# Kernel optimization log

Measured on AMD Instinct MI355X. Metric: run time of the kernel, lower is better.

The kernel has to match this reference:

```python
import jax, jax.numpy as jnp
import numpy as np

BETA = 0.25
EPS = 1e-12

def normalise(x):
    # L2 normalise over last axis
    return x / jnp.sqrt(jnp.sum(x * x, axis=-1, keepdims=True) + EPS)

def setup_inputs() -> dict:
    key = jax.random.key(0)
    k = jax.random.split(key, 6)
    N, d, c, P = 8192, 768, 256, 16384
    return {
        "z": jax.random.normal(k[0], (N, d), dtype=jnp.float32),
        "W_in": jax.random.normal(k[1], (d, c), dtype=jnp.float32) * 0.02,
        "b_in": jnp.zeros((c,), dtype=jnp.float32),
        "W_out": jax.random.normal(k[2], (c, d), dtype=jnp.float32) * 0.02,
        "b_out": jnp.zeros((d,), dtype=jnp.float32),
        "codebook": jax.random.normal(k[3], (P, c), dtype=jnp.float32),
    }

def reference(z, W_in, b_in, W_out, b_out, codebook):
    sg = jax.lax.stop_gradient
    # input projection + L2 normalise
    zq = normalise(z @ W_in + b_in)                 # [N, c]
    cb = normalise(codebook)                        # [P, c]
    # squared euclidean distances: ||z||^2 - 2 z.c + ||c||^2
    dist = (jnp.sum(zq * zq, axis=-1, keepdims=True)
            - 2.0 * jnp.einsum('nc,pc->np', zq, cb)
            + jnp.sum(cb * cb, axis=-1)[None, :])   # [N, P]
    idxes = jnp.argmin(dist, axis=-1)               # [N]
    codes = normalise(codebook[idxes])              # gather + normalise, [N, c]
    loss = BETA * (zq - sg(codes)) ** 2 + (sg(zq) - codes) ** 2
    # straight-through estimator
    codes = zq + sg(codes - zq)
    out = codes @ W_out + b_out                     # [N, d]
    return out, loss, idxes
```

## Files before the change

kernel.cpp:

```cpp
#include <hip/hip_runtime.h>
#include <hip/hip_fp16.h>
#include <math.h>

#define NN 8192
#define DD 768
#define CC 256
#define PP 16384
#define NG 256
#define MARGIN 5.0e-3f
#define BETA_C 1.25f
#define EPS_C 1e-12f

typedef __attribute__((ext_vector_type(8))) _Float16 f16x8;
typedef __attribute__((ext_vector_type(8))) short bf16x8;
typedef __attribute__((ext_vector_type(4))) float f32x4;
typedef __attribute__((ext_vector_type(16))) float f32x16;

static __device__ __forceinline__ ushort f2h(float x) {
    _Float16 h = (_Float16)x;
    return __builtin_bit_cast(unsigned short, h);
}
static __device__ __forceinline__ ushort f2bf(float x) {
    unsigned u = __float_as_uint(x);
    return (ushort)((u + 0x7fffu + ((u >> 16) & 1u)) >> 16);
}

static __device__ __forceinline__ void gload_lds16(const void* g, void* l) {
    __builtin_amdgcn_global_load_lds(
        (const __attribute__((address_space(1))) unsigned int*)g,
        (__attribute__((address_space(3))) unsigned int*)l, 16, 0, 0);
}

__global__ __launch_bounds__(256) void k_gemm_in(const float* __restrict__ z,
    const float* __restrict__ W, const float* __restrict__ b,
    float* __restrict__ zq)
{
    __shared__ float zt[64][36];
    __shared__ float wt[32][68];
    const int t = threadIdx.x;
    const int ti = t >> 4, tj = t & 15;
    const int n0 = blockIdx.x * 64;
    const int c0 = blockIdx.y * 64;

    f32x4 acc[4];
#pragma unroll
    for (int r = 0; r < 4; ++r) acc[r] = (f32x4){0.f, 0.f, 0.f, 0.f};

    for (int k0 = 0; k0 < DD; k0 += 32) {
        __syncthreads();
#pragma unroll
        for (int l = 0; l < 2; ++l) {
            int idx = l * 256 + t;
            int row = idx >> 3, c4 = idx & 7;
            *reinterpret_cast<float4*>(&zt[row][c4 * 4]) =
                *reinterpret_cast<const float4*>(&z[(size_t)(n0 + row) * DD + k0 + c4 * 4]);
            int krow = idx >> 4, w4 = idx & 15;
            *reinterpret_cast<float4*>(&wt[krow][w4 * 4]) =
                *reinterpret_cast<const float4*>(&W[(size_t)(k0 + krow) * CC + c0 + w4 * 4]);
        }
        __syncthreads();
#pragma unroll
        for (int kk = 0; kk < 32; kk += 4) {
            float4 a4[4], b4[4];
#pragma unroll
            for (int r = 0; r < 4; ++r)
                a4[r] = *reinterpret_cast<const float4*>(&zt[ti * 4 + r][kk]);
#pragma unroll
            for (int q = 0; q < 4; ++q)
                b4[q] = *reinterpret_cast<const float4*>(&wt[kk + q][tj * 4]);
#pragma unroll
            for (int q = 0; q < 4; ++q)
#pragma unroll
                for (int r = 0; r < 4; ++r) {
                    float av = ((const float*)&a4[r])[q];
                    acc[r].x += av * b4[q].x;
                    acc[r].y += av * b4[q].y;
                    acc[r].z += av * b4[q].z;
                    acc[r].w += av * b4[q].w;
                }
        }
    }
#pragma unroll
    for (int r = 0; r < 4; ++r) {
        int col = c0 + tj * 4;
        float4 o;
        o.x = acc[r].x + b[col];
        o.y = acc[r].y + b[col + 1];
        o.z = acc[r].z + b[col + 2];
        o.w = acc[r].w + b[col + 3];
        *reinterpret_cast<float4*>(&zq[(size_t)(n0 + ti * 4 + r) * CC + col]) = o;
    }
}

__global__ __launch_bounds__(256) void k_norm2(const float* __restrict__ src,
    float* __restrict__ dstf32, ushort* __restrict__ dsth, int rows)
{
    const int wave = threadIdx.x >> 6;
    const int lane = threadIdx.x & 63;
    const int row = blockIdx.x * 4 + wave;
    if (row >= rows) return;
    float4 v = *reinterpret_cast<const float4*>(&src[(size_t)row * CC + lane * 4]);
    float s = v.x * v.x + v.y * v.y + v.z * v.z + v.w * v.w;
#pragma unroll
    for (int off = 32; off; off >>= 1) s += __shfl_xor(s, off, 64);
    float r = 1.0f / sqrtf(s + EPS_C);
    v.x *= r; v.y *= r; v.z *= r; v.w *= r;
    *reinterpret_cast<float4*>(&dstf32[(size_t)row * CC + lane * 4]) = v;
    ushort4 hv;
    hv.x = f2h(v.x); hv.y = f2h(v.y); hv.z = f2h(v.z); hv.w = f2h(v.w);
    *reinterpret_cast<ushort4*>(&dsth[(size_t)row * CC + lane * 4]) = hv;
}

__global__ __launch_bounds__(256) void k_prep(const float* __restrict__ codebook,
    ushort* __restrict__ cbh, float* __restrict__ cz2, float* __restrict__ rinv,
    const float* __restrict__ W, ushort* __restrict__ wthi)
{
    __shared__ float tile[64][68];
    const int t = threadIdx.x;
    if (blockIdx.x < 4096) {
        const int wave = t >> 6;
        const int lane = t & 63;
        const int row = blockIdx.x * 4 + wave;
        float4 v = *reinterpret_cast<const float4*>(&codebook[(size_t)row * CC + lane * 4]);
        float s = v.x * v.x + v.y * v.y + v.z * v.z + v.w * v.w;
#pragma unroll
        for (int off = 32; off; off >>= 1) s += __shfl_xor(s, off, 64);
        float r = 1.0f / sqrtf(s + EPS_C);
        v.x *= r; v.y *= r; v.z *= r; v.w *= r;
        ushort4 hv;
        hv.x = f2h(v.x); hv.y = f2h(v.y); hv.z = f2h(v.z); hv.w = f2h(v.w);
        *reinterpret_cast<ushort4*>(&cbh[(size_t)row * CC + lane * 4]) = hv;
        float s2 = v.x * v.x + v.y * v.y + v.z * v.z + v.w * v.w;
#pragma unroll
        for (int off = 32; off; off >>= 1) s2 += __shfl_xor(s2, off, 64);
        if (lane == 0) {
            cz2[row] = s2;
            rinv[row] = r;
        }
    } else {
        const int id = blockIdx.x - 4096;
        const int d0 = (id % 12) * 64;
        const int k0 = (id / 12) * 64;
#pragma unroll
        for (int i = 0; i < 16; ++i) {
            int row = i * 4 + (t >> 6);
            int col = t & 63;
            tile[row][col] = W[(size_t)(k0 + row) * DD + d0 + col];
        }
        __syncthreads();
#pragma unroll
        for (int i = 0; i < 16; ++i) {
            int drow = i * 4 + (t >> 6);
            int kc = t & 63;
            wthi[(size_t)(d0 + drow) * CC + k0 + kc] = f2bf(tile[kc][drow]);
        }
    }
}

__global__ __launch_bounds__(256) void k_dist(
    const ushort* __restrict__ cbh, const ushort* __restrict__ zqh,
    const float* __restrict__ cz2,
    float* __restrict__ gmin, unsigned long long* __restrict__ maskA)
{
    __shared__ ushort lds[2][12288];
    const int t = threadIdx.x;
    const int lane = t & 63;
    const int w = t >> 6;
    const int wr = w >> 1;
    const int wc = w & 1;
    const int p0 = blockIdx.x * 256;
    const int n0 = blockIdx.y * 128;
    const int kh = lane >> 5;
    const int r31 = lane & 31;

    f32x16 acc[4][2];
#pragma unroll
    for (int mi = 0; mi < 4; ++mi) {
        const int pbm = p0 + wr * 128 + mi * 32;
#pragma unroll
        for (int q = 0; q < 4; ++q) {
            float4 cz = *reinterpret_cast<const float4*>(&cz2[pbm + q * 8 + kh * 4]);
#pragma unroll
            for (int j = 0; j < 4; ++j) {
                float v = -0.5f * ((const float*)&cz.x)[j];
                acc[mi][0][q * 4 + j] = v;
                acc[mi][1][q * 4 + j] = v;
            }
        }
    }

    const int u_l = lane >> 3;
    const int e = (lane & 7) ^ u_l;
    const int hh = e >> 2, jj = e & 3;
    const ushort* srcA[4];
    const ushort* srcB[2];
#pragma unroll
    for (int i = 0; i < 4; ++i)
        srcA[i] = cbh + (size_t)(p0 + 2 * (w * 32 + i * 8 + u_l) + hh) * CC + jj * 8;
#pragma unroll
    for (int i = 0; i < 2; ++i)
        srcB[i] = zqh + (size_t)(n0 + 2 * (w * 16 + i * 8 + u_l) + hh) * CC + jj * 8;

#define STAGE(BUF, KT)                                                        \
    {                                                                         \
        _Pragma("unroll")                                                     \
        for (int i = 0; i < 4; ++i)                                           \
            gload_lds16(srcA[i] + (KT) * 32, &lds[BUF][(w * 32 + i * 8) * 64]); \
        _Pragma("unroll")                                                     \
        for (int i = 0; i < 2; ++i)                                           \
            gload_lds16(srcB[i] + (KT) * 32, &lds[BUF][8192 + (w * 16 + i * 8) * 64]); \
    }

    const int ua = wr * 64 + (r31 >> 1);
    const int ub = wc * 32 + (r31 >> 1);
    const int hb = (r31 & 1) * 4 + kh;

#define COMPUTE(BUF)                                                          \
    {                                                                         \
        _Pragma("unroll")                                                     \
        for (int ks = 0; ks < 2; ++ks) {                                      \
            f16x8 af[4], bfv[2];                                              \
            _Pragma("unroll")                                                 \
            for (int mi = 0; mi < 4; ++mi) {                                  \
                int u = ua + mi * 16;                                         \
                af[mi] = *reinterpret_cast<const f16x8*>(                     \
                    &lds[BUF][u * 64 + (((hb + ks * 2) ^ (u & 7)) * 8)]);     \
            }                                                                 \
            _Pragma("unroll")                                                 \
            for (int ni = 0; ni < 2; ++ni) {                                  \
                int u = ub + ni * 16;                                         \
                bfv[ni] = *reinterpret_cast<const f16x8*>(                    \
                    &lds[BUF][8192 + u * 64 + (((hb + ks * 2) ^ (u & 7)) * 8)]); \
            }                                                                 \
            __builtin_amdgcn_s_setprio(1);                                    \
            acc[0][0] = __builtin_amdgcn_mfma_f32_32x32x16_f16(af[0], bfv[0], acc[0][0], 0, 0, 0); \
            acc[0][1] = __builtin_amdgcn_mfma_f32_32x32x16_f16(af[0], bfv[1], acc[0][1], 0, 0, 0); \
            acc[1][0] = __builtin_amdgcn_mfma_f32_32x32x16_f16(af[1], bfv[0], acc[1][0], 0, 0, 0); \
            acc[1][1] = __builtin_amdgcn_mfma_f32_32x32x16_f16(af[1], bfv[1], acc[1][1], 0, 0, 0); \
            acc[2][0] = __builtin_amdgcn_mfma_f32_32x32x16_f16(af[2], bfv[0], acc[2][0], 0, 0, 0); \
            acc[2][1] = __builtin_amdgcn_mfma_f32_32x32x16_f16(af[2], bfv[1], acc[2][1], 0, 0, 0); \
            acc[3][0] = __builtin_amdgcn_mfma_f32_32x32x16_f16(af[3], bfv[0], acc[3][0], 0, 0, 0); \
            acc[3][1] = __builtin_amdgcn_mfma_f32_32x32x16_f16(af[3], bfv[1], acc[3][1], 0, 0, 0); \
            __builtin_amdgcn_s_setprio(0);                                    \
        }                                                                     \
    }

#define BODY(KT, VM, DOSTAGE)                                                 \
    {                                                                         \
        if (DOSTAGE) STAGE(((KT) + 1) & 1, (KT) + 1);                         \
        __builtin_amdgcn_sched_barrier(0);                                    \
        asm volatile("s_waitcnt vmcnt(" #VM ")" ::: "memory");                \
        __builtin_amdgcn_s_barrier();                                         \
        __builtin_amdgcn_sched_barrier(0);                                    \
        COMPUTE((KT) & 1);                                                    \
        if ((KT) < 7) __builtin_amdgcn_s_barrier();                           \
    }

    STAGE(0, 0);
    BODY(0, 6, 1)
    BODY(1, 6, 1)
    BODY(2, 6, 1)
    BODY(3, 6, 1)
    BODY(4, 6, 1)
    BODY(5, 6, 1)
    BODY(6, 6, 1)
    BODY(7, 0, 0)

#undef BODY
#undef COMPUTE
#undef STAGE

#pragma unroll
    for (int ni = 0; ni < 2; ++ni) {
#pragma unroll
        for (int g = 0; g < 2; ++g) {
            float M = -1e30f;
#pragma unroll
            for (int m2 = 0; m2 < 2; ++m2)
#pragma unroll
                for (int r = 0; r < 16; ++r) M = fmaxf(M, acc[g * 2 + m2][ni][r]);
            M = fmaxf(M, __shfl_xor(M, 32, 64));
            const float thr = M - 0.5f * MARGIN;
            unsigned long long msk = 0ull;
#pragma unroll
            for (int m2 = 0; m2 < 2; ++m2)
#pragma unroll
                for (int q = 0; q < 4; ++q) {
                    unsigned nib = 0u;
#pragma unroll
                    for (int j = 0; j < 4; ++j)
                        nib |= (acc[g * 2 + m2][ni][q * 4 + j] >= thr) ? (1u << j) : 0u;
                    msk |= (unsigned long long)nib << (m2 * 32 + q * 8 + kh * 4);
                }
            msk |= __shfl_xor(msk, 32, 64);
            if (kh == 0) {
                int n = n0 + wc * 64 + ni * 32 + r31;
                int grp = (p0 >> 6) + wr * 2 + g;
                gmin[(size_t)n * NG + grp] = -2.0f * M;
                maskA[(size_t)n * NG + grp] = msk;
            }
        }
    }
}

__global__ __launch_bounds__(256) void k_pick(
    const float* __restrict__ gmin, const unsigned long long* __restrict__ maskA,
    const float* __restrict__ zqn, const float* __restrict__ cb_raw,
    const float* __restrict__ rinv, const float* __restrict__ cz2,
    float* __restrict__ idxf, ushort* __restrict__ chi, float* __restrict__ loss)
{
    __shared__ int lst[4][256];
    __shared__ int cnt[4];
    const int t = threadIdx.x;
    const int w = t >> 6;
    const int lane = t & 63;
    const int row = blockIdx.x * 4 + w;

    float4 zr = *reinterpret_cast<const float4*>(&zqn[(size_t)row * CC + lane * 4]);
    float4 gv = *reinterpret_cast<const float4*>(&gmin[(size_t)row * NG + lane * 4]);

    float pm = fminf(fminf(gv.x, gv.y), fminf(gv.z, gv.w));
#pragma unroll
    for (int off = 1; off < 64; off <<= 1) pm = fminf(pm, __shfl_xor(pm, off, 64));
    const float thresh = pm + MARGIN;

    if (lane == 0) cnt[w] = 0;
    __syncthreads();
    {
        const float g4[4] = {gv.x, gv.y, gv.z, gv.w};
#pragma unroll
        for (int j = 0; j < 4; ++j)
            if (g4[j] <= thresh) {
                int pos = atomicAdd(&cnt[w], 1);
                lst[w][pos] = lane * 4 + j;
            }
    }
    __syncthreads();

    const int nc = cnt[w];
    unsigned long long best = ~0ull;
    for (int ci = 0; ci < nc; ++ci) {
        int g = lst[w][ci];
        unsigned long long msk = maskA[(size_t)row * NG + g];
        while (msk) {
            int bit = __ffsll((long long)msk) - 1;
            msk &= msk - 1;
            int p = g * 64 + bit;
            float rv = rinv[p];
            float4 c4 = *reinterpret_cast<const float4*>(&cb_raw[(size_t)p * CC + lane * 4]);
            float part = (c4.x * rv) * zr.x + (c4.y * rv) * zr.y
                       + (c4.z * rv) * zr.z + (c4.w * rv) * zr.w;
#pragma unroll
            for (int off = 1; off < 64; off <<= 1) part += __shfl_xor(part, off, 64);
            float d4 = fmaf(-2.0f, part, 4.0f + cz2[p]);
            unsigned long long pk = ((unsigned long long)__float_as_uint(d4) << 32) | (unsigned)p;
            best = best < pk ? best : pk;
        }
    }
    const int p = (int)(best & 0xffffffffu);
    if (lane == 0) idxf[row] = (float)p;

    const float rv = rinv[p];
    float4 cv = *reinterpret_cast<const float4*>(&cb_raw[(size_t)p * CC + lane * 4]);
    cv.x *= rv; cv.y *= rv; cv.z *= rv; cv.w *= rv;
    ushort4 hv;
    hv.x = f2bf(cv.x); hv.y = f2bf(cv.y); hv.z = f2bf(cv.z); hv.w = f2bf(cv.w);
    *reinterpret_cast<ushort4*>(&chi[(size_t)row * CC + lane * 4]) = hv;
    float4 lsv;
    float dx = zr.x - cv.x, dy = zr.y - cv.y, dz = zr.z - cv.z, dw = zr.w - cv.w;
    lsv.x = BETA_C * dx * dx; lsv.y = BETA_C * dy * dy;
    lsv.z = BETA_C * dz * dz; lsv.w = BETA_C * dw * dw;
    *reinterpret_cast<float4*>(&loss[(size_t)row * CC + lane * 4]) = lsv;
}

__global__ __launch_bounds__(256) void k_gemm_out_mfma(
    const ushort* __restrict__ chi, const ushort* __restrict__ wthi,
    const float* __restrict__ bout, float* __restrict__ out)
{
    __shared__ ushort sAh[128 * 64];
    __shared__ ushort sBh[128 * 64];
    const int t = threadIdx.x;
    const int lane = t & 63;
    const int w = t >> 6;
    const int wr = w >> 1;
    const int wc = w & 1;
    const int nb = blockIdx.x * 128;
    const int db = blockIdx.y * 128;
    const int kh = lane >> 5;
    const int r31 = lane & 31;

    f32x16 acc[2][2];
#pragma unroll
    for (int mi = 0; mi < 2; ++mi)
#pragma unroll
        for (int ni = 0; ni < 2; ++ni)
#pragma unroll
            for (int r = 0; r < 16; ++r) acc[mi][ni][r] = 0.f;

    const int srow = lane >> 3;
    const int schunk = (lane & 7) ^ srow;
    const size_t rowA = (size_t)(nb + w * 32 + srow) * CC;
    const size_t rowB = (size_t)(db + w * 32 + srow) * CC;
    const char* sAhsrc = (const char*)chi + rowA * 2 + schunk * 16;
    const char* sBhsrc = (const char*)wthi + rowB * 2 + schunk * 16;
    char* dA = (char*)sAh + (w * 32) * 128;
    char* dB = (char*)sBh + (w * 32) * 128;

    const int sx = (r31 & 7) << 4;

    for (int k0 = 0; k0 < CC; k0 += 64) {
        __syncthreads();
#pragma unroll
        for (int i = 0; i < 4; ++i) {
            gload_lds16(sAhsrc + (size_t)i * 8 * (CC * 2) + k0 * 2, dA + i * 1024);
            gload_lds16(sBhsrc + (size_t)i * 8 * (CC * 2) + k0 * 2, dB + i * 1024);
        }
        __syncthreads();
#pragma unroll
        for (int ks = 0; ks < 4; ++ks) {
            const int ko = ((ks * 32 + kh * 16) ^ sx);
            bf16x8 ah[2], bh[2];
#pragma unroll
            for (int mi = 0; mi < 2; ++mi)
                ah[mi] = *reinterpret_cast<const bf16x8*>(
                    (const char*)sAh + (wr * 64 + mi * 32 + r31) * 128 + ko);
#pragma unroll
            for (int ni = 0; ni < 2; ++ni)
                bh[ni] = *reinterpret_cast<const bf16x8*>(
                    (const char*)sBh + (wc * 64 + ni * 32 + r31) * 128 + ko);
#pragma unroll
            for (int mi = 0; mi < 2; ++mi)
#pragma unroll
                for (int ni = 0; ni < 2; ++ni)
                    acc[mi][ni] = __builtin_amdgcn_mfma_f32_32x32x16_bf16(
                        ah[mi], bh[ni], acc[mi][ni], 0, 0, 0);
        }
    }

#pragma unroll
    for (int ni = 0; ni < 2; ++ni) {
        const int d = db + wc * 64 + ni * 32 + r31;
        const float bv = bout[d];
#pragma unroll
        for (int mi = 0; mi < 2; ++mi) {
            const int nbase = nb + wr * 64 + mi * 32 + 4 * kh;
#pragma unroll
            for (int q = 0; q < 4; ++q)
#pragma unroll
                for (int j = 0; j < 4; ++j) {
                    int n = nbase + j + 8 * q;
                    out[(size_t)n * DD + d] = acc[mi][ni][q * 4 + j] + bv;
                }
        }
    }
}

extern "C" void kernel_launch(void* const* d_in, const int* in_sizes, int n_in,
                              void* d_out, int out_size, void* d_ws, size_t ws_size,
                              hipStream_t stream)
{
    const float* z        = (const float*)d_in[0];
    const float* W_in     = (const float*)d_in[1];
    const float* b_in     = (const float*)d_in[2];
    const float* W_out    = (const float*)d_in[3];
    const float* b_out    = (const float*)d_in[4];
    const float* codebook = (const float*)d_in[5];

    char* ws = (char*)d_ws;
    ushort* zqh   = (ushort*)(ws);
    ushort* cbh   = (ushort*)(ws + 4194304);
    ushort* chi   = (ushort*)(ws + 12582912);
    ushort* wthi  = (ushort*)(ws + 16777216);
    float*  cz2   = (float*)(ws + 17170432);
    float*  rinv  = (float*)(ws + 17235968);

    float* out  = (float*)d_out;
    float* loss = out + (size_t)NN * DD;
    float* idxf = loss + (size_t)NN * CC;

    float* gmin = (float*)d_out;
    unsigned long long* maskA = (unsigned long long*)((char*)d_out + 8388608);
    float* zq = loss;

    k_gemm_in<<<dim3(NN / 64, CC / 64), 256, 0, stream>>>(z, W_in, b_in, zq);
    k_norm2<<<NN / 4, 256, 0, stream>>>(zq, zq, zqh, NN);
    k_prep<<<PP / 4 + 48, 256, 0, stream>>>(codebook, cbh, cz2, rinv, W_out, wthi);
    k_dist<<<dim3(PP / 256, NN / 128), 256, 0, stream>>>(cbh, zqh, cz2, gmin, maskA);
    k_pick<<<NN / 4, 256, 0, stream>>>(gmin, maskA, zq, codebook, rinv, cz2,
                                       idxf, chi, loss);
    k_gemm_out_mfma<<<dim3(NN / 128, DD / 128), 256, 0, stream>>>(chi, wthi, b_out, out);
}
```

Baseline: 177.3 us.

## Enlarge distance-kernel tile to 256x256 with 8 waves and split staging

The codebook-distance GEMM kernel now uses 512-thread blocks covering 256 codebook rows by 256 query rows, up from 256 by 128. This raises operand reuse per LDS load and halves the codebook re-reads from global memory. The grid axes are swapped so query tiles run along x. The codebook and query tile loads for the next k-step are now issued separately, one before and one between the two k-substeps, with a matching vmcnt wait count. The cost is a larger LDS footprint and more threads per block, which may lower occupancy, and the epilogue must still match the new wave layout.

```diff
diff --git a/kernel.cpp b/kernel.cpp
--- a/kernel.cpp
+++ b/kernel.cpp
@@ -157,19 +157,21 @@
     }
 }
 
-__global__ __launch_bounds__(256) void k_dist(
+__global__ __launch_bounds__(512) void k_dist(
     const ushort* __restrict__ cbh, const ushort* __restrict__ zqh,
     const float* __restrict__ cz2,
     float* __restrict__ gmin, unsigned long long* __restrict__ maskA)
 {
-    __shared__ ushort lds[2][12288];
+    __shared__ ushort lds[2][16384];
     const int t = threadIdx.x;
     const int lane = t & 63;
     const int w = t >> 6;
-    const int wr = w >> 1;
-    const int wc = w & 1;
-    const int p0 = blockIdx.x * 256;
-    const int n0 = blockIdx.y * 128;
+    const int wr = w >> 2;
+    const int wc = w & 3;
+
+    const int n0 = blockIdx.x * 256;
+    const int p0 = blockIdx.y * 256;
+
     const int kh = lane >> 5;
     const int r31 = lane & 31;
 
@@ -192,20 +194,23 @@
     const int u_l = lane >> 3;
     const int e = (lane & 7) ^ u_l;
     const int hh = e >> 2, jj = e & 3;
-    const ushort* srcA[4];
+    const ushort* srcA[2];
     const ushort* srcB[2];
 #pragma unroll
-    for (int i = 0; i < 4; ++i)
-        srcA[i] = cbh + (size_t)(p0 + 2 * (w * 32 + i * 8 + u_l) + hh) * CC + jj * 8;
+    for (int i = 0; i < 2; ++i)
+        srcA[i] = cbh + (size_t)(p0 + 2 * (w * 16 + i * 8 + u_l) + hh) * CC + jj * 8;
 #pragma unroll
     for (int i = 0; i < 2; ++i)
         srcB[i] = zqh + (size_t)(n0 + 2 * (w * 16 + i * 8 + u_l) + hh) * CC + jj * 8;
 
-#define STAGE(BUF, KT)                                                        \
+#define STAGE_A(BUF, KT)                                                      \
     {                                                                         \
         _Pragma("unroll")                                                     \
-        for (int i = 0; i < 4; ++i)                                           \
-            gload_lds16(srcA[i] + (KT) * 32, &lds[BUF][(w * 32 + i * 8) * 64]); \
+        for (int i = 0; i < 2; ++i)                                           \
+            gload_lds16(srcA[i] + (KT) * 32, &lds[BUF][(w * 16 + i * 8) * 64]); \
+    }
+#define STAGE_B(BUF, KT)                                                      \
+    {                                                                         \
         _Pragma("unroll")                                                     \
         for (int i = 0; i < 2; ++i)                                           \
             gload_lds16(srcB[i] + (KT) * 32, &lds[BUF][8192 + (w * 16 + i * 8) * 64]); \
@@ -215,60 +220,63 @@
     const int ub = wc * 32 + (r31 >> 1);
     const int hb = (r31 & 1) * 4 + kh;
 
-#define COMPUTE(BUF)                                                          \
+#define COMPUTE_KS(BUF, KS)                                                   \
     {                                                                         \
+        f16x8 af[4], bfv[2];                                                  \
         _Pragma("unroll")                                                     \
-        for (int ks = 0; ks < 2; ++ks) {                                      \
-            f16x8 af[4], bfv[2];                                              \
-            _Pragma("unroll")                                                 \
-            for (int mi = 0; mi < 4; ++mi) {                                  \
-                int u = ua + mi * 16;                                         \
-                af[mi] = *reinterpret_cast<const f16x8*>(                     \
-                    &lds[BUF][u * 64 + (((hb + ks * 2) ^ (u & 7)) * 8)]);     \
-            }                                                                 \
-            _Pragma("unroll")                                                 \
-            for (int ni = 0; ni < 2; ++ni) {                                  \
-                int u = ub + ni * 16;                                         \
-                bfv[ni] = *reinterpret_cast<const f16x8*>(                    \
-                    &lds[BUF][8192 + u * 64 + (((hb + ks * 2) ^ (u & 7)) * 8)]); \
-            }                                                                 \
-            __builtin_amdgcn_s_setprio(1);                                    \
-            acc[0][0] = __builtin_amdgcn_mfma_f32_32x32x16_f16(af[0], bfv[0], acc[0][0], 0, 0, 0); \
-            acc[0][1] = __builtin_amdgcn_mfma_f32_32x32x16_f16(af[0], bfv[1], acc[0][1], 0, 0, 0); \
-            acc[1][0] = __builtin_amdgcn_mfma_f32_32x32x16_f16(af[1], bfv[0], acc[1][0], 0, 0, 0); \
-            acc[1][1] = __builtin_amdgcn_mfma_f32_32x32x16_f16(af[1], bfv[1], acc[1][1], 0, 0, 0); \
-            acc[2][0] = __builtin_amdgcn_mfma_f32_32x32x16_f16(af[2], bfv[0], acc[2][0], 0, 0, 0); \
-            acc[2][1] = __builtin_amdgcn_mfma_f32_32x32x16_f16(af[2], bfv[1], acc[2][1], 0, 0, 0); \
-            acc[3][0] = __builtin_amdgcn_mfma_f32_32x32x16_f16(af[3], bfv[0], acc[3][0], 0, 0, 0); \
-            acc[3][1] = __builtin_amdgcn_mfma_f32_32x32x16_f16(af[3], bfv[1], acc[3][1], 0, 0, 0); \
-            __builtin_amdgcn_s_setprio(0);                                    \
+        for (int mi = 0; mi < 4; ++mi) {                                      \
+            int u = ua + mi * 16;                                             \
+            af[mi] = *reinterpret_cast<const f16x8*>(                         \
+                &lds[BUF][u * 64 + (((hb + (KS) * 2) ^ (u & 7)) * 8)]);       \
         }                                                                     \
+        _Pragma("unroll")                                                     \
+        for (int ni = 0; ni < 2; ++ni) {                                      \
+            int u = ub + ni * 16;                                             \
+            bfv[ni] = *reinterpret_cast<const f16x8*>(                        \
+                &lds[BUF][8192 + u * 64 + (((hb + (KS) * 2) ^ (u & 7)) * 8)]); \
+        }                                                                     \
+        __builtin_amdgcn_s_setprio(1);                                        \
+        acc[0][0] = __builtin_amdgcn_mfma_f32_32x32x16_f16(af[0], bfv[0], acc[0][0], 0, 0, 0); \
+        acc[0][1] = __builtin_amdgcn_mfma_f32_32x32x16_f16(af[0], bfv[1], acc[0][1], 0, 0, 0); \
+        acc[1][0] = __builtin_amdgcn_mfma_f32_32x32x16_f16(af[1], bfv[0], acc[1][0], 0, 0, 0); \
+        acc[1][1] = __builtin_amdgcn_mfma_f32_32x32x16_f16(af[1], bfv[1], acc[1][1], 0, 0, 0); \
+        acc[2][0] = __builtin_amdgcn_mfma_f32_32x32x16_f16(af[2], bfv[0], acc[2][0], 0, 0, 0); \
+        acc[2][1] = __builtin_amdgcn_mfma_f32_32x32x16_f16(af[2], bfv[1], acc[2][1], 0, 0, 0); \
+        acc[3][0] = __builtin_amdgcn_mfma_f32_32x32x16_f16(af[3], bfv[0], acc[3][0], 0, 0, 0); \
+        acc[3][1] = __builtin_amdgcn_mfma_f32_32x32x16_f16(af[3], bfv[1], acc[3][1], 0, 0, 0); \
+        __builtin_amdgcn_s_setprio(0);                                        \
     }
 
 #define BODY(KT, VM, DOSTAGE)                                                 \
     {                                                                         \
-        if (DOSTAGE) STAGE(((KT) + 1) & 1, (KT) + 1);                         \
+        if (DOSTAGE) STAGE_A(((KT) + 1) & 1, (KT) + 1);                       \
         __builtin_amdgcn_sched_barrier(0);                                    \
         asm volatile("s_waitcnt vmcnt(" #VM ")" ::: "memory");                \
         __builtin_amdgcn_s_barrier();                                         \
         __builtin_amdgcn_sched_barrier(0);                                    \
-        COMPUTE((KT) & 1);                                                    \
+        COMPUTE_KS((KT) & 1, 0);                                              \
+        __builtin_amdgcn_s_barrier();                                         \
+        if (DOSTAGE) STAGE_B(((KT) + 1) & 1, (KT) + 1);                       \
+        __builtin_amdgcn_sched_barrier(0);                                    \
+        COMPUTE_KS((KT) & 1, 1);                                              \
         if ((KT) < 7) __builtin_amdgcn_s_barrier();                           \
     }
 
-    STAGE(0, 0);
-    BODY(0, 6, 1)
-    BODY(1, 6, 1)
-    BODY(2, 6, 1)
-    BODY(3, 6, 1)
-    BODY(4, 6, 1)
-    BODY(5, 6, 1)
-    BODY(6, 6, 1)
+    STAGE_A(0, 0);
+    STAGE_B(0, 0);
+    BODY(0, 2, 1)
+    BODY(1, 2, 1)
+    BODY(2, 2, 1)
+    BODY(3, 2, 1)
+    BODY(4, 2, 1)
+    BODY(5, 2, 1)
+    BODY(6, 2, 1)
     BODY(7, 0, 0)
 
 #undef BODY
-#undef COMPUTE
-#undef STAGE
+#undef COMPUTE_KS
+#undef STAGE_A
+#undef STAGE_B
 
 #pragma unroll
     for (int ni = 0; ni < 2; ++ni) {
@@ -485,7 +493,7 @@
     k_gemm_in<<<dim3(NN / 64, CC / 64), 256, 0, stream>>>(z, W_in, b_in, zq);
     k_norm2<<<NN / 4, 256, 0, stream>>>(zq, zq, zqh, NN);
     k_prep<<<PP / 4 + 48, 256, 0, stream>>>(codebook, cbh, cz2, rinv, W_out, wthi);
-    k_dist<<<dim3(PP / 256, NN / 128), 256, 0, stream>>>(cbh, zqh, cz2, gmin, maskA);
+    k_dist<<<dim3(NN / 256, PP / 256), 512, 0, stream>>>(cbh, zqh, cz2, gmin, maskA);
     k_pick<<<NN / 4, 256, 0, stream>>>(gmin, maskA, zq, codebook, rinv, cz2,
                                        idxf, chi, loss);
     k_gemm_out_mfma<<<dim3(NN / 128, DD / 128), 256, 0, stream>>>(chi, wthi, b_out, out);
```

Result: slower. 182.6 us (+3.0%).
